# Kernel tuning notes

Hardware: AMD Instinct MI355X
Metric: run time of the kernel (lower is better)

## Reference

```python
import jax, jax.numpy as jnp
import numpy as np

N = 100000        # nodes
E = 1600000       # edges (avg degree 16)
IN_CH = 128
HID = 64
NUM_CLASSES = 40
LAYERS = 15
DT = 0.1
JACOBI_STEPS = 2


def setup_inputs() -> dict:
    key = jax.random.key(0)
    ks = jax.random.split(key, 8)
    x = jax.random.normal(ks[0], (N, IN_CH), dtype=jnp.float32)
    edge_index = jax.random.randint(ks[1], (2, E), 0, N, dtype=jnp.int32)
    s = 1.0 / np.sqrt(IN_CH)
    W_lx = jax.random.normal(ks[2], (IN_CH, HID), dtype=jnp.float32) * s
    b_lx = jnp.zeros((HID,), dtype=jnp.float32)
    W_ly = jax.random.normal(ks[3], (IN_CH, HID), dtype=jnp.float32) * s
    b_ly = jnp.zeros((HID,), dtype=jnp.float32)
    taus = jnp.full((LAYERS,), 0.7, dtype=jnp.float32)
    logit_scale = jnp.asarray(2.5, dtype=jnp.float32)
    W_ro = jax.random.normal(ks[4], (HID, NUM_CLASSES), dtype=jnp.float32) * (1.0 / np.sqrt(HID))
    b_ro = jnp.zeros((NUM_CLASSES,), dtype=jnp.float32)
    return {"x": x, "W_lx": W_lx, "b_lx": b_lx, "W_ly": W_ly, "b_ly": b_ly,
            "taus": taus, "logit_scale": logit_scale, "W_ro": W_ro, "b_ro": b_ro,
            "edge_index": edge_index}


def reference(x, W_lx, b_lx, W_ly, b_ly, taus, logit_scale, W_ro, b_ro, edge_index):
    # Eval mode: dropout is identity. y0_mode='ones' so lift_y is unused.
    src, dst = edge_index[0], edge_index[1]
    # symmetric normalization D^-1/2 A D^-1/2 from edge list
    deg = jax.ops.segment_sum(jnp.ones((E,), dtype=x.dtype), dst, num_segments=N)
    dinv = jax.lax.rsqrt(jnp.maximum(deg, 1.0))
    enorm = dinv[src] * dinv[dst]              # [E]

    def agg(Z):                                 # A_hat @ Z  via gather/scatter
        return jax.ops.segment_sum(enorm[:, None] * Z[src], dst, num_segments=N)

    X0 = jnp.tanh(x @ W_lx + b_lx)              # [N, HID]
    Y0 = jnp.ones_like(X0)
    h = jnp.concatenate([X0, Y0], axis=-1)      # [N, 2*HID]

    for l in range(LAYERS):
        X, Y = h[:, :HID], h[:, HID:]
        # Lotka-Volterra reaction terms
        fX = X * (1.0 - Y)
        fY = Y * (X - 1.0)
        rhs = jnp.concatenate([X + DT * fX, Y + DT * fY], axis=-1)
        # semi-implicit diffusion: ((1+dt)I - dt*A_hat) Z = rhs, Jacobi iterations
        Z = rhs
        for _ in range(JACOBI_STEPS):
            Z = (rhs + DT * agg(Z)) / (1.0 + DT)
        tau = jax.nn.sigmoid(taus[l])
        h = (1.0 - tau) * h + tau * Z

    Xout = h[:, :HID]
    return (logit_scale * Xout) @ W_ro + b_ro   # [N, NUM_CLASSES]
```

## Files before the change

### kernel.cpp

```cpp
#include <hip/hip_runtime.h>

#define DT_C   0.1f
#define INV1P  0.9090909090909091f


__device__ __forceinline__ unsigned bf16rne(float f) {
  unsigned b = __float_as_uint(f);
  return (b + 0x7fffu + ((b >> 16) & 1u)) >> 16;
}
__device__ __forceinline__ unsigned packbf(float x, float y) {
  return bf16rne(x) | (bf16rne(y) << 16);
}


#if __has_builtin(__builtin_amdgcn_cvt_pk_fp8_f32) && __has_builtin(__builtin_amdgcn_cvt_pk_f32_fp8)
typedef float vf2 __attribute__((ext_vector_type(2)));
__device__ __forceinline__ unsigned pk4_fp8(float a, float b, float c, float d) {
  int v = __builtin_amdgcn_cvt_pk_fp8_f32(a, b, 0, false);
  v = __builtin_amdgcn_cvt_pk_fp8_f32(c, d, v, true);
  return (unsigned)v;
}
__device__ __forceinline__ void unpk4_fp8(unsigned v, float& a, float& b, float& c, float& d) {
  vf2 lo = __builtin_amdgcn_cvt_pk_f32_fp8((int)v, false);
  vf2 hi = __builtin_amdgcn_cvt_pk_f32_fp8((int)v, true);
  a = lo[0]; b = lo[1]; c = hi[0]; d = hi[1];
}
#else
__device__ __forceinline__ unsigned enc8(float f) {
  unsigned u = __float_as_uint(f);
  unsigned mag = u & 0x7fffffffu;
  if (mag > 0x43E00000u) mag = 0x43E00000u;
  unsigned r = mag + 0x7FFFFu + ((mag >> 20) & 1u);
  int e8 = (int)(r >> 23) - 120;
  unsigned code = 0;
  if (e8 > 0) code = ((unsigned)(e8 > 15 ? 15 : e8) << 3) | ((r >> 20) & 7u);
  return code | ((u >> 24) & 0x80u);
}
__device__ __forceinline__ float dec8(unsigned c) {
  unsigned e = (c >> 3) & 15u, m = c & 7u, s = (c & 0x80u) << 24;
  if (e == 0) return __uint_as_float(s);
  return __uint_as_float(s | ((e + 120u) << 23) | (m << 20));
}
__device__ __forceinline__ unsigned pk4_fp8(float a, float b, float c, float d) {
  return enc8(a) | (enc8(b) << 8) | (enc8(c) << 16) | (enc8(d) << 24);
}
__device__ __forceinline__ void unpk4_fp8(unsigned v, float& a, float& b, float& c, float& d) {
  a = dec8(v & 0xffu); b = dec8((v >> 8) & 0xffu);
  c = dec8((v >> 16) & 0xffu); d = dec8(v >> 24);
}
#endif


__global__ __launch_bounds__(256) void k_deg(const int* __restrict__ dst,
                                             int* __restrict__ deg, int e) {
  int i = blockIdx.x * 256 + threadIdx.x;
  if (i < e) atomicAdd(&deg[dst[i]], 1);
}

__global__ __launch_bounds__(256) void k_dinv(const int* __restrict__ deg,
                                              float* __restrict__ dinv, int n) {
  int i = blockIdx.x * 256 + threadIdx.x;
  if (i < n) {
    float d = (float)deg[i];
    dinv[i] = rsqrtf(fmaxf(d, 1.0f));
  }
}

__global__ __launch_bounds__(1024) void k_scanA(const int* __restrict__ deg,
                                                int* __restrict__ rowptr,
                                                int* __restrict__ bsum, int n) {
  __shared__ int sm[1024];
  int t = threadIdx.x;
  int i = blockIdx.x * 1024 + t;
  int v = (i < n) ? deg[i] : 0;
  sm[t] = v;
  __syncthreads();
  for (int off = 1; off < 1024; off <<= 1) {
    int u = (t >= off) ? sm[t - off] : 0;
    __syncthreads();
    sm[t] += u;
    __syncthreads();
  }
  if (i < n) rowptr[i] = sm[t] - v;
  if (t == 1023) bsum[blockIdx.x] = sm[t];
}

__global__ __launch_bounds__(1024) void k_scanB(int* __restrict__ bsum, int g) {
  __shared__ int sm[1024];
  int t = threadIdx.x;
  int v = (t < g) ? bsum[t] : 0;
  sm[t] = v;
  __syncthreads();
  for (int off = 1; off < 1024; off <<= 1) {
    int u = (t >= off) ? sm[t - off] : 0;
    __syncthreads();
    sm[t] += u;
    __syncthreads();
  }
  if (t < g) bsum[t] = sm[t] - v;
}

__global__ __launch_bounds__(1024) void k_scanC(int* __restrict__ rowptr,
                                                const int* __restrict__ bsum,
                                                int n, int etot) {
  int i = blockIdx.x * 1024 + threadIdx.x;
  if (i < n) rowptr[i] += bsum[blockIdx.x];
  if (i == 0) rowptr[n] = etot;
}

__global__ __launch_bounds__(256) void k_fill(const int* __restrict__ src,
                                              const int* __restrict__ dst,
                                              const int* __restrict__ rowptr,
                                              int* __restrict__ deg,
                                              const float* __restrict__ dinv,
                                              unsigned* __restrict__ csr, int e) {
  int i = blockIdx.x * 256 + threadIdx.x;
  if (i >= e) return;
  int s = src[i], d = dst[i];
  int pos = rowptr[d] + atomicSub(&deg[d], 1) - 1;
  unsigned wb = __float_as_uint(dinv[s] * dinv[d]);
  wb = (wb + 0x10000u) & 0xFFFE0000u;
  csr[pos] = wb | (unsigned)s;
}


__global__ __launch_bounds__(256) void k_gemm_in(const float* __restrict__ x,
                                                 const float* __restrict__ Wlx,
                                                 const float* __restrict__ blx,
                                                 unsigned* __restrict__ h_b,
                                                 unsigned* __restrict__ rhs8,
                                                 int n, int ntiles) {
  __shared__ float xs[16 * 128];
  int t = threadIdx.x;
  int lane = t & 63;
  int wib  = t >> 6;
  unsigned wp[64];
#pragma unroll
  for (int j = 0; j < 64; ++j)
    wp[j] = packbf(Wlx[(2 * j) * 64 + lane], Wlx[(2 * j + 1) * 64 + lane]);
  float bl = blx[lane];

  for (int tile = blockIdx.x; tile < ntiles; tile += gridDim.x) {
    int base = tile * 16;
    __syncthreads();
    for (int v = t; v < 512; v += 256) {
      long idx = (long)base * 128 + v * 4;
      float4 val = {0.f, 0.f, 0.f, 0.f};
      if (idx < (long)n * 128) val = *(const float4*)(x + idx);
      *(float4*)(xs + v * 4) = val;
    }
    __syncthreads();
    for (int r = 0; r < 4; ++r) {
      int row = base + wib * 4 + r;
      if (row < n) {
        const float* xr = &xs[(wib * 4 + r) * 128];
        float acc = bl;
#pragma unroll
        for (int j = 0; j < 32; ++j) {
          float4 xv = *(const float4*)(xr + j * 4);
          unsigned p0 = wp[2 * j], p1 = wp[2 * j + 1];
          acc = fmaf(xv.x, __uint_as_float(p0 << 16),         acc);
          acc = fmaf(xv.y, __uint_as_float(p0 & 0xffff0000u), acc);
          acc = fmaf(xv.z, __uint_as_float(p1 << 16),         acc);
          acc = fmaf(xv.w, __uint_as_float(p1 & 0xffff0000u), acc);
        }
        float X0 = tanhf(acc);
        float a = __shfl(X0, (2 * lane) & 63);
        float b = __shfl(X0, (2 * lane + 1) & 63);
        unsigned hw = (lane < 32) ? packbf(a, b) : 0x3f803f80u;
        h_b[(size_t)row * 64 + lane] = hw;
        int b4 = (lane < 16) ? 4 * lane : 4 * (lane - 16);
        float v0 = __shfl(X0, (b4 + 0) & 63);
        float v1 = __shfl(X0, (b4 + 1) & 63);
        float v2 = __shfl(X0, (b4 + 2) & 63);
        float v3 = __shfl(X0, (b4 + 3) & 63);
        if (lane >= 16) {
          v0 = 1.f + DT_C * (v0 - 1.f);
          v1 = 1.f + DT_C * (v1 - 1.f);
          v2 = 1.f + DT_C * (v2 - 1.f);
          v3 = 1.f + DT_C * (v3 - 1.f);
        }
        unsigned pw = pk4_fp8(v0, v1, v2, v3);
        if (lane < 32) rhs8[(size_t)row * 32 + lane] = pw;
      }
    }
  }
}


__device__ __forceinline__ void gather8(const unsigned* __restrict__ Zb8,
                                        const unsigned* __restrict__ csr,
                                        int beg, int end, int g, int q,
                                        float acc[8]) {
#pragma unroll
  for (int i = 0; i < 8; ++i) acc[i] = 0.f;
  int last = end - 1;
  const uint2* Z2 = (const uint2*)Zb8;
  for (int e0 = beg; e0 < end; e0 += 16) {
    unsigned c[4]; float wk[4]; uint2 u[4];
#pragma unroll
    for (int k = 0; k < 4; ++k) {
      int idx = e0 + 4 * k + g;
      int ic  = (idx < end) ? idx : last;
      c[k]  = csr[ic];
      wk[k] = (idx < end) ? __uint_as_float(c[k] & 0xFFFE0000u) : 0.f;
    }
#pragma unroll
    for (int k = 0; k < 4; ++k)
      u[k] = Z2[(size_t)(c[k] & 0x1FFFFu) * 16 + q];
#pragma unroll
    for (int k = 0; k < 4; ++k) {
      float f0, f1, f2, f3, f4, f5, f6, f7;
      unpk4_fp8(u[k].x, f0, f1, f2, f3);
      unpk4_fp8(u[k].y, f4, f5, f6, f7);
      acc[0] = fmaf(wk[k], f0, acc[0]);
      acc[1] = fmaf(wk[k], f1, acc[1]);
      acc[2] = fmaf(wk[k], f2, acc[2]);
      acc[3] = fmaf(wk[k], f3, acc[3]);
      acc[4] = fmaf(wk[k], f4, acc[4]);
      acc[5] = fmaf(wk[k], f5, acc[5]);
      acc[6] = fmaf(wk[k], f6, acc[6]);
      acc[7] = fmaf(wk[k], f7, acc[7]);
    }
  }
#pragma unroll
  for (int i = 0; i < 8; ++i) {
    acc[i] += __shfl_xor(acc[i], 16);
    acc[i] += __shfl_xor(acc[i], 32);
  }
}


__global__ __launch_bounds__(256) void k_aggA(const unsigned* __restrict__ rhs8,
                                              unsigned* __restrict__ Z18,
                                              const int* __restrict__ rowptr,
                                              const unsigned* __restrict__ csr, int n) {
  int node = __builtin_amdgcn_readfirstlane((blockIdx.x * 256 + threadIdx.x) >> 6);
  if (node >= n) return;
  int lane = threadIdx.x & 63;
  int g = lane >> 4, q = lane & 15;
  int beg = __builtin_amdgcn_readfirstlane(rowptr[node]);
  int end = __builtin_amdgcn_readfirstlane(rowptr[node + 1]);

  uint2 rr = ((const uint2*)rhs8)[(size_t)node * 16 + q];

  float acc[8];
  gather8(rhs8, csr, beg, end, g, q, acc);

  float r8[8];
  unpk4_fp8(rr.x, r8[0], r8[1], r8[2], r8[3]);
  unpk4_fp8(rr.y, r8[4], r8[5], r8[6], r8[7]);
  if (g == 0) {
    uint2 o;
    o.x = pk4_fp8((r8[0] + DT_C * acc[0]) * INV1P, (r8[1] + DT_C * acc[1]) * INV1P,
                  (r8[2] + DT_C * acc[2]) * INV1P, (r8[3] + DT_C * acc[3]) * INV1P);
    o.y = pk4_fp8((r8[4] + DT_C * acc[4]) * INV1P, (r8[5] + DT_C * acc[5]) * INV1P,
                  (r8[6] + DT_C * acc[6]) * INV1P, (r8[7] + DT_C * acc[7]) * INV1P);
    ((uint2*)Z18)[(size_t)node * 16 + q] = o;
  }
}


__device__ __forceinline__ void rch_from_h(const uint4 hb, int q,
                                           float hv[8], float rch[8]) {
  unsigned hw[4] = {hb.x, hb.y, hb.z, hb.w};
#pragma unroll
  for (int i = 0; i < 4; ++i) {
    hv[2 * i]     = __uint_as_float(hw[i] << 16);
    hv[2 * i + 1] = __uint_as_float(hw[i] & 0xffff0000u);
  }
  float pv[8];
#pragma unroll
  for (int i = 0; i < 8; ++i) pv[i] = __shfl_xor(hv[i], 8);
  bool isX = (q < 8);
#pragma unroll
  for (int i = 0; i < 8; ++i)
    rch[i] = isX ? hv[i] + DT_C * hv[i] * (1.0f - pv[i])
                 : hv[i] + DT_C * hv[i] * (pv[i] - 1.0f);
}

__global__ __launch_bounds__(256) void k_aggB(const unsigned* __restrict__ Z18,
                                              unsigned* __restrict__ rhs8,
                                              unsigned* __restrict__ h_b,
                                              const int* __restrict__ rowptr,
                                              const unsigned* __restrict__ csr,
                                              const float* __restrict__ taus,
                                              int layer, int n) {
  int node = __builtin_amdgcn_readfirstlane((blockIdx.x * 256 + threadIdx.x) >> 6);
  if (node >= n) return;
  int lane = threadIdx.x & 63;
  int g = lane >> 4, q = lane & 15;
  int beg = __builtin_amdgcn_readfirstlane(rowptr[node]);
  int end = __builtin_amdgcn_readfirstlane(rowptr[node + 1]);

  uint4 hb = *((const uint4*)(h_b + (size_t)node * 64) + q);
  float hv[8], rch[8];
  rch_from_h(hb, q, hv, rch);

  float acc[8];
  gather8(Z18, csr, beg, end, g, q, acc);

  float tv  = taus[layer];
  float tau = 1.0f / (1.0f + expf(-tv));
  float hnew[8];
#pragma unroll
  for (int i = 0; i < 8; ++i) {
    float z = (rch[i] + DT_C * acc[i]) * INV1P;
    hnew[i] = (1.0f - tau) * hv[i] + tau * z;
  }
  if (g == 0) {
    uint4 o;
    o.x = packbf(hnew[0], hnew[1]);
    o.y = packbf(hnew[2], hnew[3]);
    o.z = packbf(hnew[4], hnew[5]);
    o.w = packbf(hnew[6], hnew[7]);
    *((uint4*)(h_b + (size_t)node * 64) + q) = o;
  }
  float pn[8];
#pragma unroll
  for (int i = 0; i < 8; ++i) pn[i] = __shfl_xor(hnew[i], 8);
  bool isX = (q < 8);
  float rn[8];
#pragma unroll
  for (int i = 0; i < 8; ++i)
    rn[i] = isX ? hnew[i] + DT_C * hnew[i] * (1.0f - pn[i])
                : hnew[i] + DT_C * hnew[i] * (pn[i] - 1.0f);
  if (g == 0) {
    uint2 o;
    o.x = pk4_fp8(rn[0], rn[1], rn[2], rn[3]);
    o.y = pk4_fp8(rn[4], rn[5], rn[6], rn[7]);
    ((uint2*)rhs8)[(size_t)node * 16 + q] = o;
  }
}


__global__ __launch_bounds__(256) void k_gemm_out(const unsigned* __restrict__ h_b,
                                                  const float* __restrict__ Wro,
                                                  const float* __restrict__ bro,
                                                  const float* __restrict__ lscale,
                                                  float* __restrict__ out, int n) {
  __shared__ float ws[64 * 40];
  __shared__ float xs[16 * 64];
  int t = threadIdx.x;
  for (int i = t; i < 64 * 40; i += 256) ws[i] = Wro[i];
  int base = blockIdx.x * 16;
  for (int v = t; v < 512; v += 256) {
    int rr = v >> 5;
    int wq = v & 31;
    int row = base + rr;
    float a = 0.f, b = 0.f;
    if (row < n) {
      unsigned u = h_b[(size_t)row * 64 + wq];
      a = __uint_as_float(u << 16);
      b = __uint_as_float(u & 0xffff0000u);
    }
    xs[rr * 64 + 2 * wq]     = a;
    xs[rr * 64 + 2 * wq + 1] = b;
  }
  __syncthreads();
  float ls = *lscale;
  int lane = t & 63;
  int wib  = t >> 6;
  float bb = (lane < 40) ? bro[lane] : 0.f;
  for (int r = 0; r < 4; ++r) {
    int row = base + wib * 4 + r;
    if (row < n && lane < 40) {
      const float* xr = &xs[(wib * 4 + r) * 64];
      float acc = 0.f;
#pragma unroll
      for (int k = 0; k < 64; ++k) acc = fmaf(xr[k], ws[k * 40 + lane], acc);
      out[row * 40 + lane] = ls * acc + bb;
    }
  }
}


extern "C" void kernel_launch(void* const* d_in, const int* in_sizes, int n_in,
                              void* d_out, int out_size, void* d_ws, size_t ws_size,
                              hipStream_t stream) {
  const float* x     = (const float*)d_in[0];
  const float* Wlx   = (const float*)d_in[1];
  const float* blx   = (const float*)d_in[2];
  const float* taus  = (const float*)d_in[5];
  const float* lsc   = (const float*)d_in[6];
  const float* Wro   = (const float*)d_in[7];
  const float* bro   = (const float*)d_in[8];
  const int*   eidx  = (const int*)d_in[9];
  int n = in_sizes[0] / 128;
  int e = in_sizes[9] / 2;
  const int* srcp = eidx;
  const int* dstp = eidx + e;
  float* out = (float*)d_out;

  char* ws = (char*)d_ws;
  size_t off = 0;
  auto alloc = [&](size_t bytes) -> void* {
    void* p = ws + off;
    off += (bytes + 255) & ~(size_t)255;
    return p;
  };
  int*      deg     = (int*)     alloc((size_t)n * 4);
  float*    dinv    = (float*)   alloc((size_t)n * 4);
  int*      rowptr  = (int*)     alloc((size_t)(n + 1) * 4);
  int*      bsum    = (int*)     alloc(1024 * 4);
  unsigned* csr     = (unsigned*)alloc((size_t)e * 4);
  unsigned* h_b     = (unsigned*)alloc((size_t)n * 64 * 4);
  unsigned* rhs8    = (unsigned*)alloc((size_t)n * 32 * 4);
  unsigned* Z18     = (unsigned*)alloc((size_t)n * 32 * 4);
  (void)ws_size; (void)n_in; (void)out_size;

  (void)hipMemsetAsync(deg, 0, (size_t)n * 4, stream);

  int eb = (e + 255) / 256;
  int sb = (n + 1023) / 1024;
  k_deg <<<eb, 256, 0, stream>>>(dstp, deg, e);
  k_dinv<<<(n + 255) / 256, 256, 0, stream>>>(deg, dinv, n);
  k_scanA<<<sb, 1024, 0, stream>>>(deg, rowptr, bsum, n);
  k_scanB<<<1, 1024, 0, stream>>>(bsum, sb);
  k_scanC<<<sb, 1024, 0, stream>>>(rowptr, bsum, n, e);
  k_fill<<<eb, 256, 0, stream>>>(srcp, dstp, rowptr, deg, dinv, csr, e);

  int ntiles = (n + 15) / 16;
  int gb = ntiles < 2048 ? ntiles : 2048;
  k_gemm_in<<<gb, 256, 0, stream>>>(x, Wlx, blx, h_b, rhs8, n, ntiles);

  int ab = (n * 64 + 255) / 256;
  for (int l = 0; l < 15; ++l) {
    k_aggA<<<ab, 256, 0, stream>>>(rhs8, Z18, rowptr, csr, n);
    k_aggB<<<ab, 256, 0, stream>>>(Z18, rhs8, h_b, rowptr, csr, taus, l, n);
  }

  k_gemm_out<<<(n + 15) / 16, 256, 0, stream>>>(h_b, Wro, bro, lsc, out, n);
}
```

Baseline: 1.576 ms.

## Use bf16 MFMA for input GEMM and fold dinv into scan kernel

Rewrites the input projection GEMM to convert x tiles to bf16 in shared memory and compute with 16x16x32 bf16 MFMA instructions, replacing the per-lane scalar FMA loop that held the weights in registers. The weights are staged transposed in padded shared memory, and the epilogue is rebuilt with xor shuffles to pack the h and fp8 rhs outputs. The dinv computation is merged into the first scan kernel, removing one launch, and the GEMM grid is capped at 1024 blocks. This also rounds the activations x to bf16 before the multiply, which adds precision loss that was not there before.

```diff
diff --git a/kernel.cpp b/kernel.cpp
--- a/kernel.cpp
+++ b/kernel.cpp
@@ -2,6 +2,9 @@
 
 #define DT_C   0.1f
 #define INV1P  0.9090909090909091f
+
+typedef short bf16x8 __attribute__((ext_vector_type(8)));
+typedef float f32x4  __attribute__((ext_vector_type(4)));
 
 
 __device__ __forceinline__ unsigned bf16rne(float f) {
@@ -57,22 +60,15 @@
   if (i < e) atomicAdd(&deg[dst[i]], 1);
 }
 
-__global__ __launch_bounds__(256) void k_dinv(const int* __restrict__ deg,
-                                              float* __restrict__ dinv, int n) {
-  int i = blockIdx.x * 256 + threadIdx.x;
-  if (i < n) {
-    float d = (float)deg[i];
-    dinv[i] = rsqrtf(fmaxf(d, 1.0f));
-  }
-}
-
 __global__ __launch_bounds__(1024) void k_scanA(const int* __restrict__ deg,
                                                 int* __restrict__ rowptr,
-                                                int* __restrict__ bsum, int n) {
+                                                int* __restrict__ bsum,
+                                                float* __restrict__ dinv, int n) {
   __shared__ int sm[1024];
   int t = threadIdx.x;
   int i = blockIdx.x * 1024 + t;
   int v = (i < n) ? deg[i] : 0;
+  if (i < n) dinv[i] = rsqrtf(fmaxf((float)v, 1.0f));
   sm[t] = v;
   __syncthreads();
   for (int off = 1; off < 1024; off <<= 1) {
@@ -124,66 +120,88 @@
 }
 
 
+#define WPAD 72
+
 __global__ __launch_bounds__(256) void k_gemm_in(const float* __restrict__ x,
                                                  const float* __restrict__ Wlx,
                                                  const float* __restrict__ blx,
                                                  unsigned* __restrict__ h_b,
                                                  unsigned* __restrict__ rhs8,
                                                  int n, int ntiles) {
-  __shared__ float xs[16 * 128];
+  __shared__ unsigned wt[64 * WPAD];
+  __shared__ unsigned xb[16 * WPAD];
   int t = threadIdx.x;
   int lane = t & 63;
   int wib  = t >> 6;
-  unsigned wp[64];
-#pragma unroll
-  for (int j = 0; j < 64; ++j)
-    wp[j] = packbf(Wlx[(2 * j) * 64 + lane], Wlx[(2 * j + 1) * 64 + lane]);
-  float bl = blx[lane];
+  int ml = lane & 15;
+  int kg = lane >> 4;
+  int nb = wib * 16;
+  int c  = nb + ml;
+
+  for (int i = t; i < 4096; i += 256) {
+    int nc = i & 63, kp = i >> 6;
+    wt[nc * WPAD + kp] = packbf(Wlx[(2 * kp) * 64 + nc], Wlx[(2 * kp + 1) * 64 + nc]);
+  }
+  float bl = blx[c];
+  __syncthreads();
 
   for (int tile = blockIdx.x; tile < ntiles; tile += gridDim.x) {
     int base = tile * 16;
-    __syncthreads();
-    for (int v = t; v < 512; v += 256) {
-      long idx = (long)base * 128 + v * 4;
-      float4 val = {0.f, 0.f, 0.f, 0.f};
-      if (idx < (long)n * 128) val = *(const float4*)(x + idx);
-      *(float4*)(xs + v * 4) = val;
-    }
-    __syncthreads();
-    for (int r = 0; r < 4; ++r) {
-      int row = base + wib * 4 + r;
-      if (row < n) {
-        const float* xr = &xs[(wib * 4 + r) * 128];
-        float acc = bl;
-#pragma unroll
-        for (int j = 0; j < 32; ++j) {
-          float4 xv = *(const float4*)(xr + j * 4);
-          unsigned p0 = wp[2 * j], p1 = wp[2 * j + 1];
-          acc = fmaf(xv.x, __uint_as_float(p0 << 16),         acc);
-          acc = fmaf(xv.y, __uint_as_float(p0 & 0xffff0000u), acc);
-          acc = fmaf(xv.z, __uint_as_float(p1 << 16),         acc);
-          acc = fmaf(xv.w, __uint_as_float(p1 & 0xffff0000u), acc);
+    for (int i = t; i < 1024; i += 256) {
+      int r = i >> 6, kp = i & 63;
+      unsigned pw = 0;
+      if (base + r < n) {
+        float2 f = *(const float2*)(x + (size_t)(base + r) * 128 + 2 * kp);
+        pw = packbf(f.x, f.y);
+      }
+      xb[r * WPAD + kp] = pw;
+    }
+    __syncthreads();
+
+    f32x4 acc = {bl, bl, bl, bl};
+#pragma unroll
+    for (int kk = 0; kk < 4; ++kk) {
+      bf16x8 a = *(const bf16x8*)&xb[ml * WPAD + kk * 16 + kg * 4];
+      bf16x8 b = *(const bf16x8*)&wt[(nb + ml) * WPAD + kk * 16 + kg * 4];
+      acc = __builtin_amdgcn_mfma_f32_16x16x32_bf16(a, b, acc, 0, 0, 0);
+    }
+
+    float tv[4], u1[4], u2[4], u3[4];
+#pragma unroll
+    for (int j = 0; j < 4; ++j) tv[j] = tanhf(acc[j]);
+#pragma unroll
+    for (int j = 0; j < 4; ++j) {
+      u1[j] = __shfl_xor(tv[j], 1);
+      u2[j] = __shfl_xor(tv[j], 2);
+      u3[j] = __shfl_xor(u1[j], 2);
+    }
+    if ((ml & 1) == 0) {
+#pragma unroll
+      for (int j = 0; j < 4; ++j) {
+        int row = base + kg * 4 + j;
+        if (row < n) h_b[(size_t)row * 64 + (c >> 1)] = packbf(tv[j], u1[j]);
+      }
+    } else {
+#pragma unroll
+      for (int j = 0; j < 4; ++j) {
+        int row = base + kg * 4 + j;
+        if (row < n) h_b[(size_t)row * 64 + 32 + (c >> 1)] = 0x3f803f80u;
+      }
+    }
+    if ((ml & 3) == 0) {
+      int wq = c >> 2;
+#pragma unroll
+      for (int j = 0; j < 4; ++j) {
+        int row = base + kg * 4 + j;
+        if (row < n) {
+          rhs8[(size_t)row * 32 + wq] = pk4_fp8(tv[j], u1[j], u2[j], u3[j]);
+          rhs8[(size_t)row * 32 + 16 + wq] =
+              pk4_fp8(1.f + DT_C * (tv[j] - 1.f), 1.f + DT_C * (u1[j] - 1.f),
+                      1.f + DT_C * (u2[j] - 1.f), 1.f + DT_C * (u3[j] - 1.f));
         }
-        float X0 = tanhf(acc);
-        float a = __shfl(X0, (2 * lane) & 63);
-        float b = __shfl(X0, (2 * lane + 1) & 63);
-        unsigned hw = (lane < 32) ? packbf(a, b) : 0x3f803f80u;
-        h_b[(size_t)row * 64 + lane] = hw;
-        int b4 = (lane < 16) ? 4 * lane : 4 * (lane - 16);
-        float v0 = __shfl(X0, (b4 + 0) & 63);
-        float v1 = __shfl(X0, (b4 + 1) & 63);
-        float v2 = __shfl(X0, (b4 + 2) & 63);
-        float v3 = __shfl(X0, (b4 + 3) & 63);
-        if (lane >= 16) {
-          v0 = 1.f + DT_C * (v0 - 1.f);
-          v1 = 1.f + DT_C * (v1 - 1.f);
-          v2 = 1.f + DT_C * (v2 - 1.f);
-          v3 = 1.f + DT_C * (v3 - 1.f);
-        }
-        unsigned pw = pk4_fp8(v0, v1, v2, v3);
-        if (lane < 32) rhs8[(size_t)row * 32 + lane] = pw;
       }
     }
+    __syncthreads();
   }
 }
 
@@ -414,14 +432,13 @@
   int eb = (e + 255) / 256;
   int sb = (n + 1023) / 1024;
   k_deg <<<eb, 256, 0, stream>>>(dstp, deg, e);
-  k_dinv<<<(n + 255) / 256, 256, 0, stream>>>(deg, dinv, n);
-  k_scanA<<<sb, 1024, 0, stream>>>(deg, rowptr, bsum, n);
+  k_scanA<<<sb, 1024, 0, stream>>>(deg, rowptr, bsum, dinv, n);
   k_scanB<<<1, 1024, 0, stream>>>(bsum, sb);
   k_scanC<<<sb, 1024, 0, stream>>>(rowptr, bsum, n, e);
   k_fill<<<eb, 256, 0, stream>>>(srcp, dstp, rowptr, deg, dinv, csr, e);
 
   int ntiles = (n + 15) / 16;
-  int gb = ntiles < 2048 ? ntiles : 2048;
+  int gb = ntiles < 1024 ? ntiles : 1024;
   k_gemm_in<<<gb, 256, 0, stream>>>(x, Wlx, blx, h_b, rhs8, n, ntiles);
 
   int ab = (n * 64 + 255) / 256;
```

Result: faster. 1.537 ms (median of 2 runs) (-2.5%).
